# Kernel tuning notes

Hardware: AMD Instinct MI355X
Metric: run time of the kernel (lower is better)

Reference implementation:

```python
import jax, jax.numpy as jnp
import numpy as np


def setup_inputs() -> dict:
    key = jax.random.key(0)
    ks = jax.random.split(key, 5)
    B, in_ch, H, W = 8, 256, 128, 128
    C = in_ch // 4
    x = jax.random.normal(ks[0], (B, in_ch, H, W), dtype=jnp.float32)
    # 1x1 conv weights stored as [out_ch, in_ch] (kernel spatial dims are 1)
    w_in = jax.random.normal(ks[1], (C, in_ch), dtype=jnp.float32) * (1.0 / np.sqrt(in_ch))
    b_in = jax.random.normal(ks[2], (C,), dtype=jnp.float32) * 0.01
    w_out = jax.random.normal(ks[3], (in_ch, C), dtype=jnp.float32) * (1.0 / np.sqrt(C))
    b_out = jax.random.normal(ks[4], (in_ch,), dtype=jnp.float32) * 0.01
    detal = jnp.array([0.1], dtype=jnp.float32)
    return {"x": x, "w_in": w_in, "b_in": b_in, "w_out": w_out, "b_out": b_out, "detal": detal}


def _mda(x, w_in, b_in, w_out, b_out, detal):
    # InConv: 1x1 conv == channel GEMM
    inp = jnp.einsum('bihw,oi->bohw', x, w_in) + b_in[None, :, None, None]
    B, C, H, W = inp.shape

    # ---- W branch ----
    # AdaptiveAvgPool2d((None,1)) -> mean over W; softmax over size-1 axis (== ones, kept for faithfulness)
    f_w = jax.nn.softmax(inp.mean(axis=3, keepdims=True), axis=3)          # [B,C,H,1]
    f_w = jnp.transpose(f_w, (0, 3, 1, 2)).reshape(B, C * H, 1)
    Xw = inp.reshape(B, C * H, W)
    Gw = Xw * f_w                                                          # [B,CH,W]
    Tw = jax.nn.softmax(jnp.einsum('bkw,bkv->bwv', Gw, Gw), axis=1)        # [B,W,W], softmax over rows
    Wo = jnp.einsum('bkw,bwv->bkv', Xw, Tw).reshape(B, C, H, W)

    # ---- H branch ----
    f_h = jax.nn.softmax(jnp.transpose(inp, (0, 1, 3, 2)).mean(axis=3, keepdims=True), axis=3)  # [B,C,W,1]
    f_h = jnp.transpose(f_h, (0, 3, 1, 2)).reshape(B, C * W, 1)
    Xh = inp.reshape(B, C * W, H)  # raw .view as in torch (scrambles H/W axes intentionally)
    Gh = Xh * f_h
    Th = jax.nn.softmax(jnp.einsum('bkh,bkg->bhg', Gh, Gh), axis=1)        # [B,H,H]
    Ho = jnp.einsum('bkh,bhg->bkg', Xh, Th).reshape(B, C, H, W)

    # ---- C branch ----
    perm = jnp.transpose(inp, (0, 2, 3, 1))                                # [B,H,W,C]
    f_c = jax.nn.softmax(perm.mean(axis=3, keepdims=True), axis=3)         # [B,H,W,1]
    f_c = jnp.transpose(f_c, (0, 3, 1, 2)).reshape(B, H * W, 1)
    Xc = perm.reshape(B, H * W, C)
    Gc = f_c * Xc
    Tc = jax.nn.softmax(jnp.einsum('bnc,bnd->bcd', Gc, Gc), axis=1)        # [B,C,C]
    # torch does .view(B,C,H,W) on a [B,H*W,C] tensor: raw reshape, NOT a transpose
    Co = jnp.einsum('bnc,bcd->bnd', Xc, Tc).reshape(B, C, H, W)

    s = detal[0] * (Co + Wo + Ho)
    # OuConv 1x1 + residual
    return jnp.einsum('bchw,oc->bohw', s, w_out) + b_out[None, :, None, None] + x


def reference(x, w_in, b_in, w_out, b_out, detal):
    return _mda(x, w_in, b_in, w_out, b_out, detal)
```

## Files before the change

### kernel.cpp

```cpp
#include <hip/hip_runtime.h>
#include <math.h>

#define NB 8
#define IC 256
#define CC 64
#define HH 128
#define WW 128
#define NN (HH*WW)
#define NKW 64
#define NKC 64

typedef _Float16 f16x8 __attribute__((ext_vector_type(8)));
typedef float f32x4 __attribute__((ext_vector_type(4)));

static constexpr size_t SZ_INP  = (size_t)NB * CC * NN;
static constexpr size_t OFF_INP = 0;
static constexpr size_t OFF_S   = OFF_INP + SZ_INP;
static constexpr size_t OFF_PC  = OFF_S + SZ_INP;
static constexpr size_t OFF_TW  = OFF_PC + (size_t)NB * NKC * 4096;
static constexpr size_t OFF_TC  = OFF_TW + (size_t)NB * 16384;
static constexpr size_t OFF_WT  = OFF_TC + (size_t)NB * 4096;
static constexpr size_t OFF_WOT = OFF_WT + 16384;
static constexpr size_t OFF_TWT = OFF_WOT + 16384;
static constexpr size_t OFF_TCT = OFF_TWT + 65536;

__global__ __launch_bounds__(256) void k_wt(
    const float* __restrict__ w_in, const float* __restrict__ w_out,
    _Float16* __restrict__ wh, _Float16* __restrict__ woh)
{
    const int idx = blockIdx.x * 256 + threadIdx.x;
    if (idx < 16384) wh[idx] = (_Float16)w_in[idx];
    else             woh[idx - 16384] = (_Float16)w_out[idx - 16384];
}

__global__ __launch_bounds__(256) void k_inconv(
    const float* __restrict__ x, const _Float16* __restrict__ wh,
    const float* __restrict__ b_in, float* __restrict__ inp)
{
    __shared__ __align__(16) _Float16 wl[64 * 264];
    __shared__ __align__(16) _Float16 xh[128 * 72];
    const int b  = blockIdx.y;
    const int n0 = blockIdx.x * 128;
    const int t  = threadIdx.x;
    const int l  = t & 63, wv = t >> 6;
    const int lr = l & 15, kg = (l >> 4) * 8;

    {
        const int r = t >> 2, c = (t & 3) * 64;
        const uint4* src = (const uint4*)(wh + r * 256 + c);
        uint4* dst = (uint4*)(wl + r * 264 + c);
#pragma unroll
        for (int k = 0; k < 8; k++) dst[k] = src[k];
    }

    f32x4 acc[4][2];
#pragma unroll
    for (int mt = 0; mt < 4; mt++)
#pragma unroll
        for (int nt = 0; nt < 2; nt++) acc[mt][nt] = (f32x4){0.f, 0.f, 0.f, 0.f};

    for (int kc = 0; kc < 4; ++kc) {
        __syncthreads();
        {
            const int nn = t & 127, ch = t >> 7;
            const float* src = x + ((size_t)b * IC + kc * 64 + ch * 32) * NN + n0 + nn;
#pragma unroll
            for (int k2 = 0; k2 < 4; ++k2) {
                float f[8];
#pragma unroll
                for (int j = 0; j < 8; ++j) f[j] = src[(size_t)(k2 * 8 + j) * NN];
                f16x8 h;
#pragma unroll
                for (int j = 0; j < 8; ++j) h[j] = (_Float16)f[j];
                *(f16x8*)(xh + nn * 72 + ch * 32 + k2 * 8) = h;
            }
        }
        __syncthreads();

#pragma unroll
        for (int kk = 0; kk < 2; ++kk) {
            f16x8 bf[2];
#pragma unroll
            for (int nt = 0; nt < 2; ++nt)
                bf[nt] = *(const f16x8*)(xh + (wv * 32 + nt * 16 + lr) * 72 + kk * 32 + kg);
#pragma unroll
            for (int mt = 0; mt < 4; ++mt) {
                const f16x8 af = *(const f16x8*)(wl + (mt * 16 + lr) * 264 + kc * 64 + kk * 32 + kg);
                acc[mt][0] = __builtin_amdgcn_mfma_f32_16x16x32_f16(af, bf[0], acc[mt][0], 0, 0, 0);
                acc[mt][1] = __builtin_amdgcn_mfma_f32_16x16x32_f16(af, bf[1], acc[mt][1], 0, 0, 0);
            }
        }
    }

#pragma unroll
    for (int mt = 0; mt < 4; ++mt)
#pragma unroll
        for (int nt = 0; nt < 2; ++nt) {
            const int n = n0 + wv * 32 + nt * 16 + lr;
#pragma unroll
            for (int r = 0; r < 4; ++r) {
                const int o = mt * 16 + (l >> 4) * 4 + r;
                inp[((size_t)b * CC + o) * NN + n] = (float)acc[mt][nt][r] + b_in[o];
            }
        }
}

__global__ __launch_bounds__(256) void k_gramW(const float* __restrict__ inp, float* __restrict__ pW)
{
    __shared__ float xs[32 * 132];
    const int b = blockIdx.y, kc = blockIdx.x;
    const int t = threadIdx.x, tx = t & 15, ty = t >> 4;
    const float* Xb = inp + (size_t)b * CC * NN;
    const int k0 = kc * ((CC * HH) / NKW);

    float acc[8][8];
#pragma unroll
    for (int i = 0; i < 8; i++)
#pragma unroll
        for (int j = 0; j < 8; j++) acc[i][j] = 0.f;

    for (int kk = k0; kk < k0 + (CC * HH) / NKW; kk += 32) {
        __syncthreads();
        {
            const int r = t >> 3, cq = (t & 7) * 16;
            const float* src = Xb + ((size_t)kk + r) * WW + cq;
            float* dst = xs + r * 132 + cq;
#pragma unroll
            for (int j = 0; j < 4; j++)
                *(float4*)(dst + 4 * j) = *(const float4*)(src + 4 * j);
        }
        __syncthreads();
#pragma unroll 8
        for (int k = 0; k < 32; k++) {
            const float* row = xs + k * 132;
            float4 t0 = *(const float4*)(row + ty * 8);
            float4 t1 = *(const float4*)(row + ty * 8 + 4);
            float4 u0 = *(const float4*)(row + tx * 8);
            float4 u1 = *(const float4*)(row + tx * 8 + 4);
            float av[8] = {t0.x, t0.y, t0.z, t0.w, t1.x, t1.y, t1.z, t1.w};
            float bv[8] = {u0.x, u0.y, u0.z, u0.w, u1.x, u1.y, u1.z, u1.w};
#pragma unroll
            for (int i = 0; i < 8; i++)
#pragma unroll
                for (int j = 0; j < 8; j++) acc[i][j] += av[i] * bv[j];
        }
    }
    float* dst = pW + ((size_t)b * NKW + kc) * 16384;
#pragma unroll
    for (int i = 0; i < 8; i++)
#pragma unroll
        for (int j = 0; j < 8; j += 4) {
            float4 v = make_float4(acc[i][j], acc[i][j + 1], acc[i][j + 2], acc[i][j + 3]);
            *(float4*)(dst + (ty * 8 + i) * 128 + tx * 8 + j) = v;
        }
}

__global__ __launch_bounds__(256) void k_redW(const float* __restrict__ pW, float* __restrict__ Tw)
{
    const int b = blockIdx.y;
    const int idx = blockIdx.x * 256 + threadIdx.x;
    const float* p = pW + (size_t)b * NKW * 16384 + idx;
    float acc = 0.f;
#pragma unroll
    for (int k = 0; k < NKW; k++) acc += p[(size_t)k * 16384];
    Tw[(size_t)b * 16384 + idx] = acc;
}

__global__ __launch_bounds__(1024) void k_softW(const float* __restrict__ Tw, _Float16* __restrict__ twt)
{
    __shared__ float red[32 * 33];
    const int b = blockIdx.x, v0 = blockIdx.y * 32;
    const int t = threadIdx.x;
    const int vc = t & 31, wg = t >> 5;
    const float* S = Tw + (size_t)b * 16384 + v0 + vc;

    float v[4];
    float m = -3.4e38f;
#pragma unroll
    for (int j = 0; j < 4; j++) { v[j] = S[(wg * 4 + j) * 128]; m = fmaxf(m, v[j]); }
    red[wg * 33 + vc] = m;
    __syncthreads();
    for (int st = 16; st > 0; st >>= 1) {
        if (wg < st) red[wg * 33 + vc] = fmaxf(red[wg * 33 + vc], red[(wg + st) * 33 + vc]);
        __syncthreads();
    }
    m = red[vc];
    __syncthreads();
    float sum = 0.f;
#pragma unroll
    for (int j = 0; j < 4; j++) { v[j] = __expf(v[j] - m); sum += v[j]; }
    red[wg * 33 + vc] = sum;
    __syncthreads();
    for (int st = 16; st > 0; st >>= 1) {
        if (wg < st) red[wg * 33 + vc] += red[(wg + st) * 33 + vc];
        __syncthreads();
    }
    const float inv = 1.f / red[vc];
    _Float16* dst = twt + (size_t)b * 16384 + (size_t)(v0 + vc) * 128 + wg * 4;
#pragma unroll
    for (int j = 0; j < 4; j++) dst[j] = (_Float16)(v[j] * inv);
}

__global__ __launch_bounds__(256) void k_gramC(const float* __restrict__ inp, float* __restrict__ pC)
{
    __shared__ float xt[32 * 68];
    const int b = blockIdx.y, nc = blockIdx.x;
    const int t = threadIdx.x, tx = t & 15, ty = t >> 4;
    const float* ip = inp + (size_t)b * CC * NN;
    const int n0 = nc * (NN / NKC);

    float acc[4][4];
#pragma unroll
    for (int i = 0; i < 4; i++)
#pragma unroll
        for (int j = 0; j < 4; j++) acc[i][j] = 0.f;

    const int scc = t >> 2;
    const int sn  = (t & 3) * 8;

    for (int nt = 0; nt < NN / NKC; nt += 32) {
        __syncthreads();
        {
            const float* src = ip + (size_t)scc * NN + n0 + nt + sn;
            float v[8];
            *(float4*)(v)     = *(const float4*)(src);
            *(float4*)(v + 4) = *(const float4*)(src + 4);
#pragma unroll
            for (int j = 0; j < 8; j++) xt[(sn + j) * 68 + scc] = v[j];
        }
        __syncthreads();
#pragma unroll 8
        for (int nn = 0; nn < 32; nn++) {
            const float4 a4 = *(const float4*)(xt + nn * 68 + ty * 4);
            const float4 e4 = *(const float4*)(xt + nn * 68 + tx * 4);
            const float av[4] = {a4.x, a4.y, a4.z, a4.w};
            const float ev[4] = {e4.x, e4.y, e4.z, e4.w};
#pragma unroll
            for (int i = 0; i < 4; i++)
#pragma unroll
                for (int j = 0; j < 4; j++) acc[i][j] += av[i] * ev[j];
        }
    }
    float* dst = pC + ((size_t)b * NKC + nc) * 4096;
#pragma unroll
    for (int i = 0; i < 4; i++) {
        float4 v = make_float4(acc[i][0], acc[i][1], acc[i][2], acc[i][3]);
        *(float4*)(dst + (ty * 4 + i) * 64 + tx * 4) = v;
    }
}

__global__ __launch_bounds__(256) void k_redC(const float* __restrict__ pC, float* __restrict__ Tc)
{
    const int b = blockIdx.y;
    const int idx = blockIdx.x * 256 + threadIdx.x;
    const float* p = pC + (size_t)b * NKC * 4096 + idx;
    float acc = 0.f;
#pragma unroll
    for (int k = 0; k < NKC; k++) acc += p[(size_t)k * 4096];
    Tc[(size_t)b * 4096 + idx] = acc;
}

__global__ __launch_bounds__(1024) void k_softC(const float* __restrict__ Tc, _Float16* __restrict__ tct)
{
    __shared__ float red[16 * 65];
    const int b = blockIdx.x;
    const int t = threadIdx.x;
    const int dc = t & 63, cg = t >> 6;
    const float* S = Tc + (size_t)b * 4096 + dc;

    float v[4];
    float m = -3.4e38f;
#pragma unroll
    for (int j = 0; j < 4; j++) { v[j] = S[(cg * 4 + j) * 64]; m = fmaxf(m, v[j]); }
    red[cg * 65 + dc] = m;
    __syncthreads();
    for (int st = 8; st > 0; st >>= 1) {
        if (cg < st) red[cg * 65 + dc] = fmaxf(red[cg * 65 + dc], red[(cg + st) * 65 + dc]);
        __syncthreads();
    }
    m = red[dc];
    __syncthreads();
    float sum = 0.f;
#pragma unroll
    for (int j = 0; j < 4; j++) { v[j] = __expf(v[j] - m); sum += v[j]; }
    red[cg * 65 + dc] = sum;
    __syncthreads();
    for (int st = 8; st > 0; st >>= 1) {
        if (cg < st) red[cg * 65 + dc] += red[(cg + st) * 65 + dc];
        __syncthreads();
    }
    const float inv = 1.f / red[dc];
    _Float16* dst = tct + (size_t)b * 4096 + (size_t)dc * 64 + cg * 4;
#pragma unroll
    for (int j = 0; j < 4; j++) dst[j] = (_Float16)(v[j] * inv);
}

__global__ __launch_bounds__(256) void k_co(
    const float* __restrict__ inp, const _Float16* __restrict__ tct,
    const float* __restrict__ detal, float* __restrict__ s)
{
    __shared__ __align__(16) _Float16 xh[128 * 72];
    __shared__ __align__(16) _Float16 tl[64 * 72];
    const int b  = blockIdx.y;
    const int n0 = blockIdx.x * 128;
    const int t  = threadIdx.x;
    const int l  = t & 63, wv = t >> 6;
    const int lr = l & 15, kg = (l >> 4) * 8;

    {
        const int nn = t & 127, ch = t >> 7;
        const float* src = inp + ((size_t)b * CC + ch * 32) * NN + n0 + nn;
#pragma unroll
        for (int k2 = 0; k2 < 4; ++k2) {
            float f[8];
#pragma unroll
            for (int j = 0; j < 8; ++j) f[j] = src[(size_t)(k2 * 8 + j) * NN];
            f16x8 h;
#pragma unroll
            for (int j = 0; j < 8; ++j) h[j] = (_Float16)f[j];
            *(f16x8*)(xh + nn * 72 + ch * 32 + k2 * 8) = h;
        }
    }
    {
        const int d = t >> 2, cq = (t & 3) * 16;
        const _Float16* src = tct + (size_t)b * 4096 + d * 64 + cq;
        *(uint4*)(tl + d * 72 + cq)     = *(const uint4*)(src);
        *(uint4*)(tl + d * 72 + cq + 8) = *(const uint4*)(src + 8);
    }
    __syncthreads();

    f32x4 acc[2][4];
#pragma unroll
    for (int mt = 0; mt < 2; mt++)
#pragma unroll
        for (int nt = 0; nt < 4; nt++) acc[mt][nt] = (f32x4){0.f, 0.f, 0.f, 0.f};

#pragma unroll
    for (int kc = 0; kc < 2; ++kc) {
        f16x8 bf[4];
#pragma unroll
        for (int nt = 0; nt < 4; ++nt)
            bf[nt] = *(const f16x8*)(tl + (nt * 16 + lr) * 72 + kc * 32 + kg);
#pragma unroll
        for (int mt = 0; mt < 2; ++mt) {
            const f16x8 af = *(const f16x8*)(xh + (wv * 32 + mt * 16 + lr) * 72 + kc * 32 + kg);
#pragma unroll
            for (int nt = 0; nt < 4; ++nt)
                acc[mt][nt] = __builtin_amdgcn_mfma_f32_16x16x32_f16(af, bf[nt], acc[mt][nt], 0, 0, 0);
        }
    }

    const float scl = detal[0];
    float* sb = s + (size_t)b * CC * NN;
#pragma unroll
    for (int mt = 0; mt < 2; ++mt)
#pragma unroll
        for (int nt = 0; nt < 4; ++nt) {
            const int d = nt * 16 + lr;
#pragma unroll
            for (int r = 0; r < 4; ++r) {
                const int n = n0 + wv * 32 + mt * 16 + (l >> 4) * 4 + r;
                sb[(size_t)n * 64 + d] = scl * acc[mt][nt][r];
            }
        }
}

__global__ __launch_bounds__(256) void k_wo(
    const float* __restrict__ inp, const _Float16* __restrict__ twt,
    const float* __restrict__ detal, float* __restrict__ s)
{
    __shared__ __align__(16) _Float16 xh[64 * 136];
    __shared__ __align__(16) _Float16 tl[128 * 136];
    const int b = blockIdx.z, hc = blockIdx.y, c = blockIdx.x;
    const int t = threadIdx.x;
    const int l = t & 63, wv = t >> 6;
    const int lr = l & 15, kg = (l >> 4) * 8;
    const int h0 = hc * 64;

    const float* ip = inp + ((size_t)b * CC + c) * NN + (size_t)h0 * WW;

    {
        const int h = t >> 2, wq = (t & 3) * 32;
        const float* src = ip + (size_t)h * WW + wq;
#pragma unroll
        for (int k2 = 0; k2 < 4; ++k2) {
            const float4 v0 = *(const float4*)(src + k2 * 8);
            const float4 v1 = *(const float4*)(src + k2 * 8 + 4);
            f16x8 h8;
            h8[0] = (_Float16)v0.x; h8[1] = (_Float16)v0.y;
            h8[2] = (_Float16)v0.z; h8[3] = (_Float16)v0.w;
            h8[4] = (_Float16)v1.x; h8[5] = (_Float16)v1.y;
            h8[6] = (_Float16)v1.z; h8[7] = (_Float16)v1.w;
            *(f16x8*)(xh + h * 136 + wq + k2 * 8) = h8;
        }
    }
    {
        const int v = t >> 1, wh2 = (t & 1) * 64;
        const _Float16* src = twt + (size_t)b * 16384 + (size_t)v * 128 + wh2;
        uint4* dst = (uint4*)(tl + v * 136 + wh2);
#pragma unroll
        for (int k = 0; k < 8; ++k) dst[k] = *(const uint4*)(src + 8 * k);
    }
    __syncthreads();

    f32x4 acc[8];
#pragma unroll
    for (int nt = 0; nt < 8; nt++) acc[nt] = (f32x4){0.f, 0.f, 0.f, 0.f};

#pragma unroll
    for (int kc = 0; kc < 4; ++kc) {
        const f16x8 af = *(const f16x8*)(xh + (wv * 16 + lr) * 136 + kc * 32 + kg);
#pragma unroll
        for (int nt = 0; nt < 8; ++nt) {
            const f16x8 bf = *(const f16x8*)(tl + (nt * 16 + lr) * 136 + kc * 32 + kg);
            acc[nt] = __builtin_amdgcn_mfma_f32_16x16x32_f16(af, bf, acc[nt], 0, 0, 0);
        }
    }

    const float sc2 = 2.0f * detal[0];
    float* sp = s + ((size_t)b * CC + c) * NN + (size_t)h0 * WW;
#pragma unroll
    for (int nt = 0; nt < 8; ++nt) {
        const int v = nt * 16 + lr;
#pragma unroll
        for (int r = 0; r < 4; ++r) {
            const int h = wv * 16 + (l >> 4) * 4 + r;
            float* p = sp + (size_t)h * WW + v;
            *p = *p + sc2 * acc[nt][r];
        }
    }
}

__global__ __launch_bounds__(256) void k_outconv(
    const float* __restrict__ s, const _Float16* __restrict__ woh,
    const float* __restrict__ b_out, const float* __restrict__ x,
    float* __restrict__ outp)
{
    __shared__ __align__(16) _Float16 wo[256 * 72];
    __shared__ __align__(16) _Float16 sh[64 * 72];
    const int b  = blockIdx.y;
    const int n0 = blockIdx.x * 64;
    const int t  = threadIdx.x;
    const int l  = t & 63, wv = t >> 6;
    const int lr = l & 15, kg = (l >> 4) * 8;

    {
        const uint4* src = (const uint4*)(woh + t * 64);
        uint4* dst = (uint4*)(wo + t * 72);
#pragma unroll
        for (int k = 0; k < 8; k++) dst[k] = src[k];
    }
    {
        const int nn = t & 63, ch = t >> 6;
        const float* src = s + ((size_t)b * CC + ch * 16) * NN + n0 + nn;
#pragma unroll
        for (int k2 = 0; k2 < 2; ++k2) {
            float f[8];
#pragma unroll
            for (int j = 0; j < 8; ++j) f[j] = src[(size_t)(k2 * 8 + j) * NN];
            f16x8 h;
#pragma unroll
            for (int j = 0; j < 8; ++j) h[j] = (_Float16)f[j];
            *(f16x8*)(sh + nn * 72 + ch * 16 + k2 * 8) = h;
        }
    }
    __syncthreads();

    f32x4 acc[4][4];
#pragma unroll
    for (int mt = 0; mt < 4; mt++)
#pragma unroll
        for (int nt = 0; nt < 4; nt++) acc[mt][nt] = (f32x4){0.f, 0.f, 0.f, 0.f};

#pragma unroll
    for (int kc = 0; kc < 2; ++kc) {
        f16x8 bf[4];
#pragma unroll
        for (int nt = 0; nt < 4; ++nt)
            bf[nt] = *(const f16x8*)(sh + (nt * 16 + lr) * 72 + kc * 32 + kg);
#pragma unroll
        for (int mt = 0; mt < 4; ++mt) {
            const f16x8 af = *(const f16x8*)(wo + (wv * 64 + mt * 16 + lr) * 72 + kc * 32 + kg);
#pragma unroll
            for (int nt = 0; nt < 4; ++nt)
                acc[mt][nt] = __builtin_amdgcn_mfma_f32_16x16x32_f16(af, bf[nt], acc[mt][nt], 0, 0, 0);
        }
    }

#pragma unroll
    for (int mt = 0; mt < 4; ++mt)
#pragma unroll
        for (int nt = 0; nt < 4; ++nt) {
            const int n = n0 + nt * 16 + lr;
#pragma unroll
            for (int r = 0; r < 4; ++r) {
                const int o = wv * 64 + mt * 16 + (l >> 4) * 4 + r;
                const size_t off = ((size_t)b * IC + o) * NN + n;
                outp[off] = (float)acc[mt][nt][r] + b_out[o] + x[off];
            }
        }
}

extern "C" void kernel_launch(void* const* d_in, const int* in_sizes, int n_in,
                              void* d_out, int out_size, void* d_ws, size_t ws_size,
                              hipStream_t stream)
{
    const float* x     = (const float*)d_in[0];
    const float* w_in  = (const float*)d_in[1];
    const float* b_in  = (const float*)d_in[2];
    const float* w_out = (const float*)d_in[3];
    const float* b_out = (const float*)d_in[4];
    const float* detal = (const float*)d_in[5];
    float* out = (float*)d_out;

    float* ws   = (float*)d_ws;
    float* inp  = ws + OFF_INP;
    float* s    = ws + OFF_S;
    float* pW   = ws + OFF_S;
    float* pC   = ws + OFF_PC;
    float* Tw   = ws + OFF_TW;
    float* Tc   = ws + OFF_TC;
    _Float16* wh  = (_Float16*)(ws + OFF_WT);
    _Float16* woh = (_Float16*)(ws + OFF_WOT);
    _Float16* twt = (_Float16*)(ws + OFF_TWT);
    _Float16* tct = (_Float16*)(ws + OFF_TCT);

    k_wt     <<<dim3(128),              256, 0, stream>>>(w_in, w_out, wh, woh);
    k_inconv <<<dim3(NN / 128, NB),     256, 0, stream>>>(x, wh, b_in, inp);
    k_gramW  <<<dim3(NKW, NB),          256, 0, stream>>>(inp, pW);
    k_redW   <<<dim3(64, NB),           256, 0, stream>>>(pW, Tw);
    k_softW  <<<dim3(NB, 4),           1024, 0, stream>>>(Tw, twt);
    k_gramC  <<<dim3(NKC, NB),          256, 0, stream>>>(inp, pC);
    k_redC   <<<dim3(16, NB),           256, 0, stream>>>(pC, Tc);
    k_softC  <<<dim3(NB),              1024, 0, stream>>>(Tc, tct);
    k_co     <<<dim3(NN / 128, NB),     256, 0, stream>>>(inp, tct, detal, s);
    k_wo     <<<dim3(CC, 2, NB),        256, 0, stream>>>(inp, twt, detal, s);
    k_outconv<<<dim3(NN / 64, NB),      256, 0, stream>>>(s, woh, b_out, x, out);
}
```

Before: 411.7 us.

## Compute W and C Gram matrices with split-fp16 MFMA instead of FP32 FMA

The W-branch and C-branch Gram kernels now split each fp32 input into high and low fp16 parts in shared memory. They accumulate with three 16x16x32 f16 MFMA instructions per tile (hi*hi, hi*lo, lo*hi), replacing scalar FP32 outer-product FMA loops. The split-K partition count drops from 64 to 32, so each block covers more K and there are fewer partials to reduce. The three-term split keeps accuracy close to fp32 at the price of extra conversion work and larger shared memory. Output stores are now scalar and strided rather than float4.

```diff
diff --git a/kernel.cpp b/kernel.cpp
--- a/kernel.cpp
+++ b/kernel.cpp
@@ -7,8 +7,8 @@
 #define HH 128
 #define WW 128
 #define NN (HH*WW)
-#define NKW 64
-#define NKC 64
+#define NKW 32
+#define NKC 32
 
 typedef _Float16 f16x8 __attribute__((ext_vector_type(8)));
 typedef float f32x4 __attribute__((ext_vector_type(4)));
@@ -107,51 +107,76 @@
 
 __global__ __launch_bounds__(256) void k_gramW(const float* __restrict__ inp, float* __restrict__ pW)
 {
-    __shared__ float xs[32 * 132];
+    __shared__ __align__(16) _Float16 xhi[128 * 72];
+    __shared__ __align__(16) _Float16 xlo[128 * 72];
     const int b = blockIdx.y, kc = blockIdx.x;
-    const int t = threadIdx.x, tx = t & 15, ty = t >> 4;
-    const float* Xb = inp + (size_t)b * CC * NN;
-    const int k0 = kc * ((CC * HH) / NKW);
-
-    float acc[8][8];
-#pragma unroll
-    for (int i = 0; i < 8; i++)
-#pragma unroll
-        for (int j = 0; j < 8; j++) acc[i][j] = 0.f;
-
-    for (int kk = k0; kk < k0 + (CC * HH) / NKW; kk += 32) {
+    const int t = threadIdx.x;
+    const int l = t & 63, wv = t >> 6;
+    const int lr = l & 15, kg = (l >> 4) * 8;
+    const float* inpb = inp + (size_t)b * CC * NN;
+    const int k0 = kc * 256;
+
+    f32x4 acc[2][8];
+#pragma unroll
+    for (int mt = 0; mt < 2; mt++)
+#pragma unroll
+        for (int nt = 0; nt < 8; nt++) acc[mt][nt] = (f32x4){0.f, 0.f, 0.f, 0.f};
+
+    for (int sub = 0; sub < 4; ++sub) {
         __syncthreads();
         {
-            const int r = t >> 3, cq = (t & 7) * 16;
-            const float* src = Xb + ((size_t)kk + r) * WW + cq;
-            float* dst = xs + r * 132 + cq;
-#pragma unroll
-            for (int j = 0; j < 4; j++)
-                *(float4*)(dst + 4 * j) = *(const float4*)(src + 4 * j);
-        }
-        __syncthreads();
-#pragma unroll 8
-        for (int k = 0; k < 32; k++) {
-            const float* row = xs + k * 132;
-            float4 t0 = *(const float4*)(row + ty * 8);
-            float4 t1 = *(const float4*)(row + ty * 8 + 4);
-            float4 u0 = *(const float4*)(row + tx * 8);
-            float4 u1 = *(const float4*)(row + tx * 8 + 4);
-            float av[8] = {t0.x, t0.y, t0.z, t0.w, t1.x, t1.y, t1.z, t1.w};
-            float bv[8] = {u0.x, u0.y, u0.z, u0.w, u1.x, u1.y, u1.z, u1.w};
-#pragma unroll
-            for (int i = 0; i < 8; i++)
-#pragma unroll
-                for (int j = 0; j < 8; j++) acc[i][j] += av[i] * bv[j];
-        }
-    }
+            const int w = t & 127, kh = (t >> 7) * 32;
+            const float* src = inpb + (size_t)(k0 + sub * 64 + kh) * 128 + w;
+#pragma unroll
+            for (int g = 0; g < 4; ++g) {
+                float f[8];
+#pragma unroll
+                for (int j = 0; j < 8; ++j) f[j] = src[(size_t)(g * 8 + j) * 128];
+                f16x8 hi, lo;
+#pragma unroll
+                for (int j = 0; j < 8; ++j) {
+                    hi[j] = (_Float16)f[j];
+                    lo[j] = (_Float16)(f[j] - (float)hi[j]);
+                }
+                *(f16x8*)(xhi + w * 72 + kh + g * 8) = hi;
+                *(f16x8*)(xlo + w * 72 + kh + g * 8) = lo;
+            }
+        }
+        __syncthreads();
+
+#pragma unroll
+        for (int kk = 0; kk < 2; ++kk) {
+            f16x8 ah[2], al[2];
+#pragma unroll
+            for (int mt = 0; mt < 2; ++mt) {
+                ah[mt] = *(const f16x8*)(xhi + (wv * 32 + mt * 16 + lr) * 72 + kk * 32 + kg);
+                al[mt] = *(const f16x8*)(xlo + (wv * 32 + mt * 16 + lr) * 72 + kk * 32 + kg);
+            }
+#pragma unroll
+            for (int nt = 0; nt < 8; ++nt) {
+                const f16x8 bh = *(const f16x8*)(xhi + (nt * 16 + lr) * 72 + kk * 32 + kg);
+                const f16x8 bl = *(const f16x8*)(xlo + (nt * 16 + lr) * 72 + kk * 32 + kg);
+#pragma unroll
+                for (int mt = 0; mt < 2; ++mt) {
+                    acc[mt][nt] = __builtin_amdgcn_mfma_f32_16x16x32_f16(ah[mt], bh, acc[mt][nt], 0, 0, 0);
+                    acc[mt][nt] = __builtin_amdgcn_mfma_f32_16x16x32_f16(ah[mt], bl, acc[mt][nt], 0, 0, 0);
+                    acc[mt][nt] = __builtin_amdgcn_mfma_f32_16x16x32_f16(al[mt], bh, acc[mt][nt], 0, 0, 0);
+                }
+            }
+        }
+    }
+
     float* dst = pW + ((size_t)b * NKW + kc) * 16384;
 #pragma unroll
-    for (int i = 0; i < 8; i++)
-#pragma unroll
-        for (int j = 0; j < 8; j += 4) {
-            float4 v = make_float4(acc[i][j], acc[i][j + 1], acc[i][j + 2], acc[i][j + 3]);
-            *(float4*)(dst + (ty * 8 + i) * 128 + tx * 8 + j) = v;
+    for (int mt = 0; mt < 2; ++mt)
+#pragma unroll
+        for (int nt = 0; nt < 8; ++nt) {
+            const int v = nt * 16 + lr;
+#pragma unroll
+            for (int r = 0; r < 4; ++r) {
+                const int w = wv * 32 + mt * 16 + (l >> 4) * 4 + r;
+                dst[(size_t)w * 128 + v] = acc[mt][nt][r];
+            }
         }
 }
 
@@ -203,49 +228,65 @@
 
 __global__ __launch_bounds__(256) void k_gramC(const float* __restrict__ inp, float* __restrict__ pC)
 {
-    __shared__ float xt[32 * 68];
+    __shared__ __align__(16) _Float16 xhi[64 * 264];
+    __shared__ __align__(16) _Float16 xlo[64 * 264];
     const int b = blockIdx.y, nc = blockIdx.x;
-    const int t = threadIdx.x, tx = t & 15, ty = t >> 4;
-    const float* ip = inp + (size_t)b * CC * NN;
-    const int n0 = nc * (NN / NKC);
-
-    float acc[4][4];
-#pragma unroll
-    for (int i = 0; i < 4; i++)
-#pragma unroll
-        for (int j = 0; j < 4; j++) acc[i][j] = 0.f;
-
-    const int scc = t >> 2;
-    const int sn  = (t & 3) * 8;
-
-    for (int nt = 0; nt < NN / NKC; nt += 32) {
+    const int t = threadIdx.x;
+    const int l = t & 63, wv = t >> 6;
+    const int lr = l & 15, kg = (l >> 4) * 8;
+    const float* inpb = inp + (size_t)b * CC * NN;
+    const int n0 = nc * 512;
+
+    f32x4 acc[4];
+#pragma unroll
+    for (int nt = 0; nt < 4; nt++) acc[nt] = (f32x4){0.f, 0.f, 0.f, 0.f};
+
+    for (int sub = 0; sub < 2; ++sub) {
         __syncthreads();
         {
-            const float* src = ip + (size_t)scc * NN + n0 + nt + sn;
-            float v[8];
-            *(float4*)(v)     = *(const float4*)(src);
-            *(float4*)(v + 4) = *(const float4*)(src + 4);
-#pragma unroll
-            for (int j = 0; j < 8; j++) xt[(sn + j) * 68 + scc] = v[j];
-        }
-        __syncthreads();
-#pragma unroll 8
-        for (int nn = 0; nn < 32; nn++) {
-            const float4 a4 = *(const float4*)(xt + nn * 68 + ty * 4);
-            const float4 e4 = *(const float4*)(xt + nn * 68 + tx * 4);
-            const float av[4] = {a4.x, a4.y, a4.z, a4.w};
-            const float ev[4] = {e4.x, e4.y, e4.z, e4.w};
-#pragma unroll
-            for (int i = 0; i < 4; i++)
-#pragma unroll
-                for (int j = 0; j < 4; j++) acc[i][j] += av[i] * ev[j];
-        }
-    }
+            const int c = t >> 2, nq = (t & 3) * 64;
+            const float* src = inpb + (size_t)c * NN + n0 + sub * 256 + nq;
+#pragma unroll
+            for (int g = 0; g < 8; ++g) {
+                const float4 v0 = *(const float4*)(src + g * 8);
+                const float4 v1 = *(const float4*)(src + g * 8 + 4);
+                float f[8] = {v0.x, v0.y, v0.z, v0.w, v1.x, v1.y, v1.z, v1.w};
+                f16x8 hi, lo;
+#pragma unroll
+                for (int j = 0; j < 8; ++j) {
+                    hi[j] = (_Float16)f[j];
+                    lo[j] = (_Float16)(f[j] - (float)hi[j]);
+                }
+                *(f16x8*)(xhi + c * 264 + nq + g * 8) = hi;
+                *(f16x8*)(xlo + c * 264 + nq + g * 8) = lo;
+            }
+        }
+        __syncthreads();
+
+#pragma unroll
+        for (int kk = 0; kk < 8; ++kk) {
+            const f16x8 ah = *(const f16x8*)(xhi + (wv * 16 + lr) * 264 + kk * 32 + kg);
+            const f16x8 al = *(const f16x8*)(xlo + (wv * 16 + lr) * 264 + kk * 32 + kg);
+#pragma unroll
+            for (int nt = 0; nt < 4; ++nt) {
+                const f16x8 bh = *(const f16x8*)(xhi + (nt * 16 + lr) * 264 + kk * 32 + kg);
+                const f16x8 bl = *(const f16x8*)(xlo + (nt * 16 + lr) * 264 + kk * 32 + kg);
+                acc[nt] = __builtin_amdgcn_mfma_f32_16x16x32_f16(ah, bh, acc[nt], 0, 0, 0);
+                acc[nt] = __builtin_amdgcn_mfma_f32_16x16x32_f16(ah, bl, acc[nt], 0, 0, 0);
+                acc[nt] = __builtin_amdgcn_mfma_f32_16x16x32_f16(al, bh, acc[nt], 0, 0, 0);
+            }
+        }
+    }
+
     float* dst = pC + ((size_t)b * NKC + nc) * 4096;
 #pragma unroll
-    for (int i = 0; i < 4; i++) {
-        float4 v = make_float4(acc[i][0], acc[i][1], acc[i][2], acc[i][3]);
-        *(float4*)(dst + (ty * 4 + i) * 64 + tx * 4) = v;
+    for (int nt = 0; nt < 4; ++nt) {
+        const int d = nt * 16 + lr;
+#pragma unroll
+        for (int r = 0; r < 4; ++r) {
+            const int c = wv * 16 + (l >> 4) * 4 + r;
+            dst[(size_t)c * 64 + d] = acc[nt][r];
+        }
     }
 }
 
```

Result: faster. 366.4 us, median of 2 (-11.0%).
